# Kernel tuning notes

Measured on AMD Instinct MI355X. Metric: run time of the kernel, lower is better.

The kernel has to match this reference:

```python
import jax, jax.numpy as jnp
import numpy as np

DIM = 1024
N = 65536

def _l2norm(x):
    # F.normalize: x / max(||x||_2, eps) along last dim, eps=1e-12
    n = jnp.linalg.norm(x, axis=-1, keepdims=True)
    return x / jnp.maximum(n, 1e-12)

def setup_inputs() -> dict:
    key = jax.random.key(0)
    ks = jax.random.split(key, 10)
    s = 0.02
    return {
        "q_init": jax.random.normal(ks[0], (1, DIM), jnp.float32),
        "k_init": jax.random.normal(ks[1], (N, DIM), jnp.float32),
        "Wq": jax.random.normal(ks[2], (DIM, DIM // 2), jnp.float32) * s,
        "bq": jnp.zeros((DIM // 2,), jnp.float32),
        "Wk": jax.random.normal(ks[3], (DIM, DIM // 2), jnp.float32) * s,
        "bk": jnp.zeros((DIM // 2,), jnp.float32),
        "Wv": jax.random.normal(ks[4], (DIM, DIM), jnp.float32) * s,
        "bv": jnp.zeros((DIM,), jnp.float32),
        "Wm": jax.random.normal(ks[5], (DIM, DIM), jnp.float32) * s,
        "bm": jnp.zeros((DIM,), jnp.float32),
        "gamma": jnp.ones((1,), jnp.float32),
    }

def reference(q_init, k_init, Wq, bq, Wk, bk, Wv, bv, Wm, bm, gamma):
    q = _l2norm(q_init) @ Wq + bq              # [1, dim/2]
    kn = _l2norm(k_init)                        # [N, dim]
    k = kn @ Wk + bk                            # [N, dim/2]
    v = kn @ Wv + bv                            # [N, dim]
    scores = q @ k.T                            # [1, N]
    # global mean/std rescale (torch.std is unbiased, ddof=1)
    scores = (scores - scores.mean()) / (jnp.std(scores, ddof=1) + 1e-8)
    attn = jax.nn.softmax(jnp.clip(scores, -10.0, 10.0), axis=-1)
    # dropout is identity in eval mode
    out = (attn @ v) @ Wm + bm                  # [1, dim]
    g = jax.nn.sigmoid(gamma)                   # [1]
    return g * q_init + (1.0 - g) * out
```

## Files before the change

### kernel.cpp

```cpp
#include <hip/hip_runtime.h>
#include <math.h>

#define DIM   1024
#define HALF  512
#define NROWS 65536
#define SBLK  4096
#define WBLK  1024
#define WF1   32

#define OFF_QN     0
#define OFF_QACC   (OFF_QN + DIM)
#define OFF_PVEC   (OFF_QACC + HALF)
#define OFF_SCAL   (OFF_PVEC + DIM)
#define OFF_PSTAT  (OFF_SCAL + 8)
#define OFF_S      (OFF_PSTAT + 2*SBLK)
#define OFF_INVN   (OFF_S + NROWS)
#define OFF_COEFF  (OFF_INVN + NROWS)
#define OFF_ESUM   (OFF_COEFF + NROWS)
#define OFF_PW     (OFF_ESUM + 256)
#define OFF_P2     (OFF_PW + WBLK*DIM)
#define OFF_WACC   (OFF_P2 + WF1*DIM)
#define OFF_OVACC  (OFF_WACC + DIM)
#define OFF_OUTACC (OFF_OVACC + DIM)
#define OFF_END    (OFF_OUTACC + DIM)

__global__ void k_qnorm(const float* __restrict__ q_init, float* __restrict__ qn) {
    __shared__ float red[1024];
    int t = threadIdx.x;
    float v = q_init[t];
    red[t] = v * v;
    __syncthreads();
    for (int s = 512; s > 0; s >>= 1) {
        if (t < s) red[t] += red[t + s];
        __syncthreads();
    }
    float inv = 1.0f / fmaxf(sqrtf(red[0]), 1e-12f);
    qn[t] = v * inv;
}

__global__ void k_matvec_col(const float* __restrict__ M,
                             const float* __restrict__ coeff,
                             const float* __restrict__ cbias,
                             float* __restrict__ out,
                             int nrows, int ncols4) {
    __shared__ float4 red[256];
    int t = threadIdx.x, c4 = blockIdx.x;
    const float4* M4 = (const float4*)M;
    float4 acc = make_float4(0.f, 0.f, 0.f, 0.f);
    for (int r = t; r < nrows; r += 256) {
        float c = coeff[r];
        if (cbias) c += cbias[r];
        float4 m = M4[(size_t)r * ncols4 + c4];
        acc.x += c * m.x; acc.y += c * m.y; acc.z += c * m.z; acc.w += c * m.w;
    }
    red[t] = acc;
    __syncthreads();
    for (int s = 128; s > 0; s >>= 1) {
        if (t < s) {
            red[t].x += red[t + s].x; red[t].y += red[t + s].y;
            red[t].z += red[t + s].z; red[t].w += red[t + s].w;
        }
        __syncthreads();
    }
    if (t == 0) ((float4*)out)[c4] = red[0];
}

__global__ void k_pvec(const float* __restrict__ Wk,
                       const float* __restrict__ qacc,
                       const float* __restrict__ bq,
                       float* __restrict__ pvec) {
    __shared__ float q[HALF];
    int t = threadIdx.x;
    for (int j = t; j < HALF; j += 256) q[j] = qacc[j] + bq[j];
    __syncthreads();
    int wave = t >> 6, lane = t & 63;
    int d = blockIdx.x * 4 + wave;
    const float* row = Wk + (size_t)d * HALF;
    float acc = 0.f;
    #pragma unroll
    for (int j0 = 0; j0 < HALF; j0 += 64) acc += row[j0 + lane] * q[j0 + lane];
    #pragma unroll
    for (int o = 32; o > 0; o >>= 1) acc += __shfl_down(acc, o);
    if (lane == 0) pvec[d] = acc;
}

__global__ void k_scores(const float* __restrict__ K,
                         const float* __restrict__ pvec,
                         float* __restrict__ svals,
                         float* __restrict__ invn,
                         float2* __restrict__ pstat) {
    __shared__ float4 p4s[256];
    __shared__ float wsum[4], wssq[4];
    int t = threadIdx.x;
    p4s[t] = ((const float4*)pvec)[t];
    __syncthreads();
    int wave = t >> 6, lane = t & 63;
    int row0 = blockIdx.x * 16 + wave * 4;
    const float4* k4 = (const float4*)K + (size_t)row0 * 256;
    float d0 = 0, d1 = 0, d2 = 0, d3 = 0;
    float q0 = 0, q1 = 0, q2 = 0, q3 = 0;
    #pragma unroll
    for (int i = 0; i < 4; ++i) {
        int idx = lane + i * 64;
        float4 p = p4s[idx];
        float4 a = k4[idx];
        float4 b = k4[256 + idx];
        float4 c = k4[512 + idx];
        float4 e = k4[768 + idx];
        d0 += a.x * p.x + a.y * p.y + a.z * p.z + a.w * p.w;
        q0 += a.x * a.x + a.y * a.y + a.z * a.z + a.w * a.w;
        d1 += b.x * p.x + b.y * p.y + b.z * p.z + b.w * p.w;
        q1 += b.x * b.x + b.y * b.y + b.z * b.z + b.w * b.w;
        d2 += c.x * p.x + c.y * p.y + c.z * p.z + c.w * p.w;
        q2 += c.x * c.x + c.y * c.y + c.z * c.z + c.w * c.w;
        d3 += e.x * p.x + e.y * p.y + e.z * p.z + e.w * p.w;
        q3 += e.x * e.x + e.y * e.y + e.z * e.z + e.w * e.w;
    }
    #pragma unroll
    for (int o = 32; o > 0; o >>= 1) {
        d0 += __shfl_down(d0, o); q0 += __shfl_down(q0, o);
        d1 += __shfl_down(d1, o); q1 += __shfl_down(q1, o);
        d2 += __shfl_down(d2, o); q2 += __shfl_down(q2, o);
        d3 += __shfl_down(d3, o); q3 += __shfl_down(q3, o);
    }
    if (lane == 0) {
        float i0 = 1.0f / fmaxf(sqrtf(q0), 1e-12f);
        float i1 = 1.0f / fmaxf(sqrtf(q1), 1e-12f);
        float i2 = 1.0f / fmaxf(sqrtf(q2), 1e-12f);
        float i3 = 1.0f / fmaxf(sqrtf(q3), 1e-12f);
        float s0 = d0 * i0, s1 = d1 * i1, s2 = d2 * i2, s3 = d3 * i3;
        float4 sv = make_float4(s0, s1, s2, s3);
        float4 iv = make_float4(i0, i1, i2, i3);
        *(float4*)(svals + row0) = sv;
        *(float4*)(invn + row0) = iv;
        wsum[wave] = s0 + s1 + s2 + s3;
        wssq[wave] = s0 * s0 + s1 * s1 + s2 * s2 + s3 * s3;
    }
    __syncthreads();
    if (t == 0)
        pstat[blockIdx.x] = make_float2(wsum[0] + wsum[1] + wsum[2] + wsum[3],
                                        wssq[0] + wssq[1] + wssq[2] + wssq[3]);
}

__global__ void k_redstats(const float2* __restrict__ pstat, float* __restrict__ scal) {
    __shared__ float rs[1024], rq[1024];
    int t = threadIdx.x;
    float s = 0.f, q = 0.f;
    for (int i = t; i < SBLK; i += 1024) {
        float2 p = pstat[i];
        s += p.x; q += p.y;
    }
    rs[t] = s; rq[t] = q;
    __syncthreads();
    for (int k = 512; k > 0; k >>= 1) {
        if (t < k) { rs[t] += rs[t + k]; rq[t] += rq[t + k]; }
        __syncthreads();
    }
    if (t == 0) {
        float mean = rs[0] / (float)NROWS;
        float var  = (rq[0] - (float)NROWS * mean * mean) / (float)(NROWS - 1);
        scal[0] = mean;
        scal[1] = 1.0f / (sqrtf(fmaxf(var, 0.0f)) + 1e-8f);
    }
}

__global__ void k_coeff(const float* __restrict__ svals,
                        const float* __restrict__ invn,
                        const float* __restrict__ scal,
                        float* __restrict__ coeff,
                        float* __restrict__ esum) {
    __shared__ float red[256];
    int t = threadIdx.x;
    int i = blockIdx.x * 256 + t;
    float mean = scal[0], rstd = scal[1];
    float z = (svals[i] - mean) * rstd;
    z = fminf(fmaxf(z, -10.0f), 10.0f);
    float e = expf(z);
    coeff[i] = e * invn[i];
    red[t] = e;
    __syncthreads();
    for (int s = 128; s > 0; s >>= 1) {
        if (t < s) red[t] += red[t + s];
        __syncthreads();
    }
    if (t == 0) esum[blockIdx.x] = red[0];
}

__global__ void k_wsum(const float* __restrict__ K,
                       const float* __restrict__ coeff,
                       float* __restrict__ pw) {
    int t = threadIdx.x;
    int r0 = blockIdx.x * 64;
    const float4* M4 = (const float4*)K + (size_t)r0 * 256 + t;
    const float* cf = coeff + r0;
    float4 acc = make_float4(0.f, 0.f, 0.f, 0.f);
    #pragma unroll 16
    for (int r = 0; r < 64; ++r) {
        float c = cf[r];
        float4 m = M4[(size_t)r * 256];
        acc.x += c * m.x; acc.y += c * m.y; acc.z += c * m.z; acc.w += c * m.w;
    }
    ((float4*)pw)[(size_t)blockIdx.x * 256 + t] = acc;
}

__global__ void k_wfold(const float* __restrict__ pw, float* __restrict__ p2) {
    int t = threadIdx.x, b = blockIdx.x;
    const float4* pw4 = (const float4*)pw;
    float4 acc = make_float4(0.f, 0.f, 0.f, 0.f);
    #pragma unroll
    for (int p = 0; p < WBLK / WF1; ++p) {
        float4 m = pw4[(size_t)(b * (WBLK / WF1) + p) * 256 + t];
        acc.x += m.x; acc.y += m.y; acc.z += m.z; acc.w += m.w;
    }
    ((float4*)p2)[b * 256 + t] = acc;
}

__global__ void k_wreduce(const float* __restrict__ p2,
                          const float* __restrict__ esum,
                          float* __restrict__ wacc) {
    __shared__ float red[256];
    int t = threadIdx.x;
    if (t < 256) red[t] = esum[t];
    __syncthreads();
    for (int s = 128; s > 0; s >>= 1) {
        if (t < s) red[t] += red[t + s];
        __syncthreads();
    }
    float inv = 1.0f / red[0];
    float acc = 0.f;
    #pragma unroll
    for (int b = 0; b < WF1; ++b) acc += p2[b * DIM + t];
    wacc[t] = acc * inv;
}

__global__ void k_final(const float* __restrict__ q_init,
                        const float* __restrict__ outacc,
                        const float* __restrict__ bm,
                        const float* __restrict__ gamma,
                        float* __restrict__ out) {
    int t = threadIdx.x;
    float g = 1.0f / (1.0f + expf(-gamma[0]));
    out[t] = g * q_init[t] + (1.0f - g) * (outacc[t] + bm[t]);
}

extern "C" void kernel_launch(void* const* d_in, const int* in_sizes, int n_in,
                              void* d_out, int out_size, void* d_ws, size_t ws_size,
                              hipStream_t stream) {
    const float* q_init = (const float*)d_in[0];
    const float* k_init = (const float*)d_in[1];
    const float* Wq     = (const float*)d_in[2];
    const float* bq     = (const float*)d_in[3];
    const float* Wk     = (const float*)d_in[4];
    const float* Wv     = (const float*)d_in[6];
    const float* bv     = (const float*)d_in[7];
    const float* Wm     = (const float*)d_in[8];
    const float* bm     = (const float*)d_in[9];
    const float* gamma  = (const float*)d_in[10];
    float* out = (float*)d_out;
    float* ws  = (float*)d_ws;

    float*  qn     = ws + OFF_QN;
    float*  qacc   = ws + OFF_QACC;
    float*  pvec   = ws + OFF_PVEC;
    float*  scal   = ws + OFF_SCAL;
    float2* pstat  = (float2*)(ws + OFF_PSTAT);
    float*  svals  = ws + OFF_S;
    float*  invn   = ws + OFF_INVN;
    float*  coeff  = ws + OFF_COEFF;
    float*  esum   = ws + OFF_ESUM;
    float*  pw     = ws + OFF_PW;
    float*  p2     = ws + OFF_P2;
    float*  wacc   = ws + OFF_WACC;
    float*  ovacc  = ws + OFF_OVACC;
    float*  outacc = ws + OFF_OUTACC;

    k_qnorm<<<1, 1024, 0, stream>>>(q_init, qn);
    k_matvec_col<<<HALF / 4, 256, 0, stream>>>(Wq, qn, nullptr, qacc, DIM, HALF / 4);
    k_pvec<<<DIM / 4, 256, 0, stream>>>(Wk, qacc, bq, pvec);
    k_scores<<<SBLK, 256, 0, stream>>>(k_init, pvec, svals, invn, pstat);
    k_redstats<<<1, 1024, 0, stream>>>(pstat, scal);
    k_coeff<<<NROWS / 256, 256, 0, stream>>>(svals, invn, scal, coeff, esum);
    k_wsum<<<WBLK, 256, 0, stream>>>(k_init, coeff, pw);
    k_wfold<<<WF1, 256, 0, stream>>>(pw, p2);
    k_wreduce<<<1, 1024, 0, stream>>>(p2, esum, wacc);
    k_matvec_col<<<DIM / 4, 256, 0, stream>>>(Wv, wacc, nullptr, ovacc, DIM, DIM / 4);
    k_matvec_col<<<DIM / 4, 256, 0, stream>>>(Wm, ovacc, bv, outacc, DIM, DIM / 4);
    k_final<<<1, 1024, 0, stream>>>(q_init, outacc, bm, gamma, out);
}
```

Baseline: 462.0 us.

## Fuse small kernels, compute softmax coefficients inside weighted sum, reverse block order

After: 472.5 us. 1.02x slower.

```diff
diff --git a/kernel.cpp b/kernel.cpp
--- a/kernel.cpp
+++ b/kernel.cpp
@@ -5,64 +5,60 @@
 #define HALF  512
 #define NROWS 65536
 #define SBLK  4096
-#define WBLK  1024
-#define WF1   32
-
-#define OFF_QN     0
-#define OFF_QACC   (OFF_QN + DIM)
+#define WBLK  2048
+#define WF1   64
+
+#define OFF_SCAL   0
+#define OFF_QACC   (OFF_SCAL + 8)
 #define OFF_PVEC   (OFF_QACC + HALF)
-#define OFF_SCAL   (OFF_PVEC + DIM)
-#define OFF_PSTAT  (OFF_SCAL + 8)
+#define OFF_PSTAT  (OFF_PVEC + DIM)
 #define OFF_S      (OFF_PSTAT + 2*SBLK)
 #define OFF_INVN   (OFF_S + NROWS)
-#define OFF_COEFF  (OFF_INVN + NROWS)
-#define OFF_ESUM   (OFF_COEFF + NROWS)
-#define OFF_PW     (OFF_ESUM + 256)
+#define OFF_PESUM  (OFF_INVN + NROWS)
+#define OFF_PW     (OFF_PESUM + WBLK)
 #define OFF_P2     (OFF_PW + WBLK*DIM)
 #define OFF_WACC   (OFF_P2 + WF1*DIM)
 #define OFF_OVACC  (OFF_WACC + DIM)
-#define OFF_OUTACC (OFF_OVACC + DIM)
-#define OFF_END    (OFF_OUTACC + DIM)
-
-__global__ void k_qnorm(const float* __restrict__ q_init, float* __restrict__ qn) {
-    __shared__ float red[1024];
-    int t = threadIdx.x;
-    float v = q_init[t];
-    red[t] = v * v;
-    __syncthreads();
-    for (int s = 512; s > 0; s >>= 1) {
+#define OFF_END    (OFF_OVACC + DIM)
+
+__global__ void k_prep(const float* __restrict__ q_init,
+                       const float* __restrict__ Wq,
+                       float* __restrict__ qacc) {
+    __shared__ float qs[DIM];
+    __shared__ float4 red4[256];
+    __shared__ float red[256];
+    int t = threadIdx.x, c4 = blockIdx.x;
+    float sq = 0.f;
+    #pragma unroll
+    for (int i = 0; i < 4; ++i) {
+        float v = q_init[t + i * 256];
+        qs[t + i * 256] = v;
+        sq += v * v;
+    }
+    red[t] = sq;
+    __syncthreads();
+    for (int s = 128; s > 0; s >>= 1) {
         if (t < s) red[t] += red[t + s];
         __syncthreads();
     }
     float inv = 1.0f / fmaxf(sqrtf(red[0]), 1e-12f);
-    qn[t] = v * inv;
-}
-
-__global__ void k_matvec_col(const float* __restrict__ M,
-                             const float* __restrict__ coeff,
-                             const float* __restrict__ cbias,
-                             float* __restrict__ out,
-                             int nrows, int ncols4) {
-    __shared__ float4 red[256];
-    int t = threadIdx.x, c4 = blockIdx.x;
-    const float4* M4 = (const float4*)M;
-    float4 acc = make_float4(0.f, 0.f, 0.f, 0.f);
-    for (int r = t; r < nrows; r += 256) {
-        float c = coeff[r];
-        if (cbias) c += cbias[r];
-        float4 m = M4[(size_t)r * ncols4 + c4];
+    const float4* W4 = (const float4*)Wq;
+    float4 acc = make_float4(0.f, 0.f, 0.f, 0.f);
+    for (int r = t; r < DIM; r += 256) {
+        float c = qs[r] * inv;
+        float4 m = W4[(size_t)r * (HALF / 4) + c4];
         acc.x += c * m.x; acc.y += c * m.y; acc.z += c * m.z; acc.w += c * m.w;
     }
-    red[t] = acc;
+    red4[t] = acc;
     __syncthreads();
     for (int s = 128; s > 0; s >>= 1) {
         if (t < s) {
-            red[t].x += red[t + s].x; red[t].y += red[t + s].y;
-            red[t].z += red[t + s].z; red[t].w += red[t + s].w;
-        }
-        __syncthreads();
-    }
-    if (t == 0) ((float4*)out)[c4] = red[0];
+            red4[t].x += red4[t + s].x; red4[t].y += red4[t + s].y;
+            red4[t].z += red4[t + s].z; red4[t].w += red4[t + s].w;
+        }
+        __syncthreads();
+    }
+    if (t == 0) ((float4*)qacc)[c4] = red4[0];
 }
 
 __global__ void k_pvec(const float* __restrict__ Wk,
@@ -96,43 +92,40 @@
     __syncthreads();
     int wave = t >> 6, lane = t & 63;
     int row0 = blockIdx.x * 16 + wave * 4;
-    const float4* k4 = (const float4*)K + (size_t)row0 * 256;
-    float d0 = 0, d1 = 0, d2 = 0, d3 = 0;
-    float q0 = 0, q1 = 0, q2 = 0, q3 = 0;
-    #pragma unroll
-    for (int i = 0; i < 4; ++i) {
-        int idx = lane + i * 64;
-        float4 p = p4s[idx];
-        float4 a = k4[idx];
-        float4 b = k4[256 + idx];
-        float4 c = k4[512 + idx];
-        float4 e = k4[768 + idx];
-        d0 += a.x * p.x + a.y * p.y + a.z * p.z + a.w * p.w;
-        q0 += a.x * a.x + a.y * a.y + a.z * a.z + a.w * a.w;
-        d1 += b.x * p.x + b.y * p.y + b.z * p.z + b.w * p.w;
-        q1 += b.x * b.x + b.y * b.y + b.z * b.z + b.w * b.w;
-        d2 += c.x * p.x + c.y * p.y + c.z * p.z + c.w * p.w;
-        q2 += c.x * c.x + c.y * c.y + c.z * c.z + c.w * c.w;
-        d3 += e.x * p.x + e.y * p.y + e.z * p.z + e.w * p.w;
-        q3 += e.x * e.x + e.y * e.y + e.z * e.z + e.w * e.w;
+    const float4* k4 = (const float4*)K + (size_t)row0 * 256 + lane;
+    float4 v[16];
+    #pragma unroll
+    for (int r = 0; r < 4; ++r)
+        #pragma unroll
+        for (int i = 0; i < 4; ++i)
+            v[r * 4 + i] = k4[r * 256 + i * 64];
+    float d[4] = {0, 0, 0, 0}, q[4] = {0, 0, 0, 0};
+    #pragma unroll
+    for (int r = 0; r < 4; ++r) {
+        #pragma unroll
+        for (int i = 0; i < 4; ++i) {
+            float4 a = v[r * 4 + i];
+            float4 p = p4s[lane + i * 64];
+            d[r] += a.x * p.x + a.y * p.y + a.z * p.z + a.w * p.w;
+            q[r] += a.x * a.x + a.y * a.y + a.z * a.z + a.w * a.w;
+        }
     }
     #pragma unroll
     for (int o = 32; o > 0; o >>= 1) {
-        d0 += __shfl_down(d0, o); q0 += __shfl_down(q0, o);
-        d1 += __shfl_down(d1, o); q1 += __shfl_down(q1, o);
-        d2 += __shfl_down(d2, o); q2 += __shfl_down(q2, o);
-        d3 += __shfl_down(d3, o); q3 += __shfl_down(q3, o);
+        #pragma unroll
+        for (int r = 0; r < 4; ++r) {
+            d[r] += __shfl_down(d[r], o);
+            q[r] += __shfl_down(q[r], o);
+        }
     }
     if (lane == 0) {
-        float i0 = 1.0f / fmaxf(sqrtf(q0), 1e-12f);
-        float i1 = 1.0f / fmaxf(sqrtf(q1), 1e-12f);
-        float i2 = 1.0f / fmaxf(sqrtf(q2), 1e-12f);
-        float i3 = 1.0f / fmaxf(sqrtf(q3), 1e-12f);
-        float s0 = d0 * i0, s1 = d1 * i1, s2 = d2 * i2, s3 = d3 * i3;
-        float4 sv = make_float4(s0, s1, s2, s3);
-        float4 iv = make_float4(i0, i1, i2, i3);
-        *(float4*)(svals + row0) = sv;
-        *(float4*)(invn + row0) = iv;
+        float i0 = 1.0f / fmaxf(sqrtf(q[0]), 1e-12f);
+        float i1 = 1.0f / fmaxf(sqrtf(q[1]), 1e-12f);
+        float i2 = 1.0f / fmaxf(sqrtf(q[2]), 1e-12f);
+        float i3 = 1.0f / fmaxf(sqrtf(q[3]), 1e-12f);
+        float s0 = d[0] * i0, s1 = d[1] * i1, s2 = d[2] * i2, s3 = d[3] * i3;
+        *(float4*)(svals + row0) = make_float4(s0, s1, s2, s3);
+        *(float4*)(invn + row0) = make_float4(i0, i1, i2, i3);
         wsum[wave] = s0 + s1 + s2 + s3;
         wssq[wave] = s0 * s0 + s1 * s1 + s2 * s2 + s3 * s3;
     }
@@ -164,43 +157,38 @@
     }
 }
 
-__global__ void k_coeff(const float* __restrict__ svals,
-                        const float* __restrict__ invn,
-                        const float* __restrict__ scal,
-                        float* __restrict__ coeff,
-                        float* __restrict__ esum) {
-    __shared__ float red[256];
-    int t = threadIdx.x;
-    int i = blockIdx.x * 256 + t;
+__global__ void k_wsum(const float* __restrict__ K,
+                       const float* __restrict__ svals,
+                       const float* __restrict__ invn,
+                       const float* __restrict__ scal,
+                       float* __restrict__ pw,
+                       float* __restrict__ pesum) {
+    int t = threadIdx.x;
+    int b = (int)gridDim.x - 1 - (int)blockIdx.x;
+    int r0 = b * 32;
     float mean = scal[0], rstd = scal[1];
-    float z = (svals[i] - mean) * rstd;
-    z = fminf(fmaxf(z, -10.0f), 10.0f);
-    float e = expf(z);
-    coeff[i] = e * invn[i];
-    red[t] = e;
-    __syncthreads();
-    for (int s = 128; s > 0; s >>= 1) {
-        if (t < s) red[t] += red[t + s];
-        __syncthreads();
-    }
-    if (t == 0) esum[blockIdx.x] = red[0];
-}
-
-__global__ void k_wsum(const float* __restrict__ K,
-                       const float* __restrict__ coeff,
-                       float* __restrict__ pw) {
-    int t = threadIdx.x;
-    int r0 = blockIdx.x * 64;
     const float4* M4 = (const float4*)K + (size_t)r0 * 256 + t;
-    const float* cf = coeff + r0;
-    float4 acc = make_float4(0.f, 0.f, 0.f, 0.f);
-    #pragma unroll 16
-    for (int r = 0; r < 64; ++r) {
-        float c = cf[r];
-        float4 m = M4[(size_t)r * 256];
-        acc.x += c * m.x; acc.y += c * m.y; acc.z += c * m.z; acc.w += c * m.w;
-    }
-    ((float4*)pw)[(size_t)blockIdx.x * 256 + t] = acc;
+    float4 acc = make_float4(0.f, 0.f, 0.f, 0.f);
+    float esum = 0.f;
+    #pragma unroll
+    for (int rb = 0; rb < 32; rb += 8) {
+        float4 m[8];
+        #pragma unroll
+        for (int r = 0; r < 8; ++r) m[r] = M4[(size_t)(rb + r) * 256];
+        #pragma unroll
+        for (int r = 0; r < 8; ++r) {
+            int ri = r0 + rb + r;
+            float z = (svals[ri] - mean) * rstd;
+            z = fminf(fmaxf(z, -10.0f), 10.0f);
+            float e = expf(z);
+            esum += e;
+            float c = e * invn[ri];
+            acc.x += c * m[r].x; acc.y += c * m[r].y;
+            acc.z += c * m[r].z; acc.w += c * m[r].w;
+        }
+    }
+    ((float4*)pw)[(size_t)b * 256 + t] = acc;
+    if (t == 0) pesum[b] = esum;
 }
 
 __global__ void k_wfold(const float* __restrict__ pw, float* __restrict__ p2) {
@@ -216,13 +204,15 @@
 }
 
 __global__ void k_wreduce(const float* __restrict__ p2,
-                          const float* __restrict__ esum,
+                          const float* __restrict__ pesum,
                           float* __restrict__ wacc) {
-    __shared__ float red[256];
-    int t = threadIdx.x;
-    if (t < 256) red[t] = esum[t];
-    __syncthreads();
-    for (int s = 128; s > 0; s >>= 1) {
+    __shared__ float red[1024];
+    int t = threadIdx.x;
+    float es = 0.f;
+    for (int i = t; i < WBLK; i += 1024) es += pesum[i];
+    red[t] = es;
+    __syncthreads();
+    for (int s = 512; s > 0; s >>= 1) {
         if (t < s) red[t] += red[t + s];
         __syncthreads();
     }
@@ -233,14 +223,68 @@
     wacc[t] = acc * inv;
 }
 
-__global__ void k_final(const float* __restrict__ q_init,
-                        const float* __restrict__ outacc,
-                        const float* __restrict__ bm,
-                        const float* __restrict__ gamma,
-                        float* __restrict__ out) {
-    int t = threadIdx.x;
-    float g = 1.0f / (1.0f + expf(-gamma[0]));
-    out[t] = g * q_init[t] + (1.0f - g) * (outacc[t] + bm[t]);
+__global__ void k_mv(const float* __restrict__ M,
+                     const float* __restrict__ coeff,
+                     const float* __restrict__ cbias,
+                     float* __restrict__ out) {
+    __shared__ float4 red[256];
+    int t = threadIdx.x, c4 = blockIdx.x;
+    const float4* M4 = (const float4*)M;
+    float4 acc = make_float4(0.f, 0.f, 0.f, 0.f);
+    for (int r = t; r < DIM; r += 256) {
+        float c = coeff[r];
+        if (cbias) c += cbias[r];
+        float4 m = M4[(size_t)r * (DIM / 4) + c4];
+        acc.x += c * m.x; acc.y += c * m.y; acc.z += c * m.z; acc.w += c * m.w;
+    }
+    red[t] = acc;
+    __syncthreads();
+    for (int s = 128; s > 0; s >>= 1) {
+        if (t < s) {
+            red[t].x += red[t + s].x; red[t].y += red[t + s].y;
+            red[t].z += red[t + s].z; red[t].w += red[t + s].w;
+        }
+        __syncthreads();
+    }
+    if (t == 0) ((float4*)out)[c4] = red[0];
+}
+
+__global__ void k_mv_final(const float* __restrict__ M,
+                           const float* __restrict__ coeff,
+                           const float* __restrict__ cbias,
+                           const float* __restrict__ q_init,
+                           const float* __restrict__ bm,
+                           const float* __restrict__ gamma,
+                           float* __restrict__ out) {
+    __shared__ float4 red[256];
+    int t = threadIdx.x, c4 = blockIdx.x;
+    const float4* M4 = (const float4*)M;
+    float4 acc = make_float4(0.f, 0.f, 0.f, 0.f);
+    for (int r = t; r < DIM; r += 256) {
+        float c = coeff[r] + cbias[r];
+        float4 m = M4[(size_t)r * (DIM / 4) + c4];
+        acc.x += c * m.x; acc.y += c * m.y; acc.z += c * m.z; acc.w += c * m.w;
+    }
+    red[t] = acc;
+    __syncthreads();
+    for (int s = 128; s > 0; s >>= 1) {
+        if (t < s) {
+            red[t].x += red[t + s].x; red[t].y += red[t + s].y;
+            red[t].z += red[t + s].z; red[t].w += red[t + s].w;
+        }
+        __syncthreads();
+    }
+    if (t == 0) {
+        float g = 1.0f / (1.0f + expf(-gamma[0]));
+        float4 qv = ((const float4*)q_init)[c4];
+        float4 bmv = ((const float4*)bm)[c4];
+        float4 o;
+        o.x = g * qv.x + (1.0f - g) * (red[0].x + bmv.x);
+        o.y = g * qv.y + (1.0f - g) * (red[0].y + bmv.y);
+        o.z = g * qv.z + (1.0f - g) * (red[0].z + bmv.z);
+        o.w = g * qv.w + (1.0f - g) * (red[0].w + bmv.w);
+        ((float4*)out)[c4] = o;
+    }
 }
 
 extern "C" void kernel_launch(void* const* d_in, const int* in_sizes, int n_in,
@@ -259,31 +303,25 @@
     float* out = (float*)d_out;
     float* ws  = (float*)d_ws;
 
-    float*  qn     = ws + OFF_QN;
+    float*  scal   = ws + OFF_SCAL;
     float*  qacc   = ws + OFF_QACC;
     float*  pvec   = ws + OFF_PVEC;
-    float*  scal   = ws + OFF_SCAL;
     float2* pstat  = (float2*)(ws + OFF_PSTAT);
     float*  svals  = ws + OFF_S;
     float*  invn   = ws + OFF_INVN;
-    float*  coeff  = ws + OFF_COEFF;
-    float*  esum   = ws + OFF_ESUM;
+    float*  pesum  = ws + OFF_PESUM;
     float*  pw     = ws + OFF_PW;
     float*  p2     = ws + OFF_P2;
     float*  wacc   = ws + OFF_WACC;
     float*  ovacc  = ws + OFF_OVACC;
-    float*  outacc = ws + OFF_OUTACC;
-
-    k_qnorm<<<1, 1024, 0, stream>>>(q_init, qn);
-    k_matvec_col<<<HALF / 4, 256, 0, stream>>>(Wq, qn, nullptr, qacc, DIM, HALF / 4);
+
+    k_prep<<<HALF / 4, 256, 0, stream>>>(q_init, Wq, qacc);
     k_pvec<<<DIM / 4, 256, 0, stream>>>(Wk, qacc, bq, pvec);
     k_scores<<<SBLK, 256, 0, stream>>>(k_init, pvec, svals, invn, pstat);
     k_redstats<<<1, 1024, 0, stream>>>(pstat, scal);
-    k_coeff<<<NROWS / 256, 256, 0, stream>>>(svals, invn, scal, coeff, esum);
-    k_wsum<<<WBLK, 256, 0, stream>>>(k_init, coeff, pw);
+    k_wsum<<<WBLK, 256, 0, stream>>>(k_init, svals, invn, scal, pw, pesum);
     k_wfold<<<WF1, 256, 0, stream>>>(pw, p2);
-    k_wreduce<<<1, 1024, 0, stream>>>(p2, esum, wacc);
-    k_matvec_col<<<DIM / 4, 256, 0, stream>>>(Wv, wacc, nullptr, ovacc, DIM, DIM / 4);
-    k_matvec_col<<<DIM / 4, 256, 0, stream>>>(Wm, ovacc, bv, outacc, DIM, DIM / 4);
-    k_final<<<1, 1024, 0, stream>>>(q_init, outacc, bm, gamma, out);
-}
+    k_wreduce<<<1, 1024, 0, stream>>>(p2, pesum, wacc);
+    k_mv<<<DIM / 4, 256, 0, stream>>>(Wv, wacc, nullptr, ovacc);
+    k_mv_final<<<DIM / 4, 256, 0, stream>>>(Wm, ovacc, bv, q_init, bm, gamma, out);
+}
```
